# Kernel optimization log

Hardware: AMD Instinct MI355X
Metric: run time of the kernel (lower is better)

Reference implementation:

```python
import jax, jax.numpy as jnp
import numpy as np

BAND_LOW_MAX = 500.0
BAND_MID_MAX = 2000.0
ENERGY_THRESHOLD = 0.5

V, NH, NM = 1024, 16384, 16384


def setup_inputs() -> dict:
    key = jax.random.key(0)
    k1, k2, k3, k4, k5, k6 = jax.random.split(key, 6)
    harm_amps = jax.random.uniform(k1, (V, NH), dtype=jnp.float32)
    noise_mags = jax.random.uniform(k2, (V, NM), dtype=jnp.float32)
    # fundamental in [50, 1000) Hz so low/mid/high bands are all populated
    f0_hz = 50.0 + 950.0 * jax.random.uniform(k3, (V,), dtype=jnp.float32)
    competition_weight = 0.1 + jax.random.uniform(k4, (V,), dtype=jnp.float32)
    withdrawal = jax.random.uniform(k5, (V, 3), dtype=jnp.float32)  # [low, mid, high]
    is_active = jax.random.randint(k6, (V,), 0, 2).astype(bool)
    return {
        'harm_amps': harm_amps,
        'noise_mags': noise_mags,
        'f0_hz': f0_hz,
        'competition_weight': competition_weight,
        'withdrawal': withdrawal,
        'is_active': is_active,
    }


def reference(harm_amps, noise_mags, f0_hz, competition_weight, withdrawal, is_active):
    dt = harm_amps.dtype
    nh = harm_amps.shape[-1]
    actf = is_active.astype(dt)                     # [V]
    n_active = jnp.sum(is_active)

    harmonics = jnp.arange(1, nh + 1, dtype=dt)     # [NH]
    freqs = f0_hz[:, None] * harmonics[None, :]     # [V, NH]
    # bands partition the harmonics: 0=low (<500), 1=mid [500,2000), 2=high (>=2000)
    band_idx = (freqs >= BAND_LOW_MAX).astype(jnp.int32) + (freqs >= BAND_MID_MAX).astype(jnp.int32)  # [V, NH]

    # per-voice per-band energy (inactive voices contribute 0, as in the torch code)
    energy = jnp.stack(
        [jnp.sum(jnp.where(band_idx == b, harm_amps, jnp.zeros((), dt)), axis=-1) for b in range(3)],
        axis=1,
    ) * actf[:, None]                               # [V, 3]

    total_energy = jnp.sum(energy, axis=0)          # [3]
    total_weight = jnp.sum(competition_weight * actf)

    claim_ratio = competition_weight / jnp.maximum(total_weight, 1e-6)  # [V]
    my_share = claim_ratio * ENERGY_THRESHOLD                           # [V]
    excess = energy - my_share[:, None]                                 # [V, 3]
    excess_ratio = excess / jnp.maximum(energy, 1e-6)                   # [V, 3]
    reduction = jnp.maximum(0.3, 1.0 - withdrawal * excess_ratio * 0.5) # [V, 3]

    # reduction only applies when band is crowded, voice has energy, and voice exceeds its share
    apply = (total_energy[None, :] > ENERGY_THRESHOLD) & (energy > 0.0) & (excess > 0.0) & is_active[:, None]
    gain = jnp.where(apply, reduction, jnp.ones((), dt))                # [V, 3]

    elem_gain = jnp.take_along_axis(gain, band_idx, axis=1)             # [V, NH]
    harm_new = harm_amps * elem_gain

    total_before = jnp.sum(harm_amps, axis=-1)      # [V]
    total_after = jnp.sum(harm_new, axis=-1)        # [V]
    noise_scale = jnp.where(total_before > 1e-6, total_after / total_before, jnp.ones((), dt))
    noise_new = noise_mags * jnp.where(is_active, noise_scale, jnp.ones((), dt))[:, None]

    # inactive voices pass through unchanged
    harm_new = jnp.where(is_active[:, None], harm_new, harm_amps)

    # fewer than 2 active voices -> no competition at all
    changed = n_active >= 2
    harm_out = jnp.where(changed, harm_new, harm_amps)
    noise_out = jnp.where(changed, noise_new, noise_mags)
    # concat harm and noise outputs along last axis: [V, NH + NM]
    return jnp.concatenate([harm_out, noise_out], axis=-1)
```

## Files before the change

### kernel.cpp

```cpp
#include <hip/hip_runtime.h>

#define V   1024
#define NH  16384
#define NM  16384

#define BAND_LOW_MAX    500.0f
#define BAND_MID_MAX    2000.0f
#define ENERGY_THRESHOLD 0.5f

__global__ __launch_bounds__(256)
void pass1_band_energy(const float* __restrict__ harm,
                       const float* __restrict__ f0_hz,
                       float* __restrict__ Eraw ) {
    const int v = blockIdx.x;
    const float f0 = f0_hz[v];
    const float4* h4 = (const float4*)(harm + (size_t)v * NH);

    float e0 = 0.f, e1 = 0.f, e2 = 0.f;
    for (int c = threadIdx.x; c < NH / 4; c += blockDim.x) {
        float4 a = h4[c];
        const int hbase = c * 4;
        #pragma unroll
        for (int j = 0; j < 4; ++j) {
            float amp  = (&a.x)[j];
            float freq = f0 * (float)(hbase + j + 1);
            if (freq < BAND_LOW_MAX)       e0 += amp;
            else if (freq < BAND_MID_MAX)  e1 += amp;
            else                           e2 += amp;
        }
    }
    for (int off = 32; off > 0; off >>= 1) {
        e0 += __shfl_down(e0, off);
        e1 += __shfl_down(e1, off);
        e2 += __shfl_down(e2, off);
    }
    __shared__ float s[3][4];
    const int wid  = threadIdx.x >> 6;
    const int lane = threadIdx.x & 63;
    if (lane == 0) { s[0][wid] = e0; s[1][wid] = e1; s[2][wid] = e2; }
    __syncthreads();
    if (threadIdx.x == 0) {
        float t0 = 0.f, t1 = 0.f, t2 = 0.f;
        #pragma unroll
        for (int i = 0; i < 4; ++i) { t0 += s[0][i]; t1 += s[1][i]; t2 += s[2][i]; }
        Eraw[v * 3 + 0] = t0;
        Eraw[v * 3 + 1] = t1;
        Eraw[v * 3 + 2] = t2;
    }
}

__global__ __launch_bounds__(1024)
void pass2_gains(const float* __restrict__ Eraw,
                 const float* __restrict__ cw,
                 const float* __restrict__ wd,
                 const int*   __restrict__ is_active,
                 float* __restrict__ gains ) {
    const int v = threadIdx.x;
    const float e0 = Eraw[v * 3 + 0];
    const float e1 = Eraw[v * 3 + 1];
    const float e2 = Eraw[v * 3 + 2];
    const bool  act  = (is_active[v] != 0);
    const float actf = act ? 1.0f : 0.0f;
    const float w    = cw[v];

    const float ea0 = e0 * actf, ea1 = e1 * actf, ea2 = e2 * actf;

    float r0 = ea0, r1 = ea1, r2 = ea2, r3 = w * actf, r4 = actf;
    for (int off = 32; off > 0; off >>= 1) {
        r0 += __shfl_down(r0, off);
        r1 += __shfl_down(r1, off);
        r2 += __shfl_down(r2, off);
        r3 += __shfl_down(r3, off);
        r4 += __shfl_down(r4, off);
    }
    __shared__ float s[5][16];
    __shared__ float tot[5];
    const int wid  = threadIdx.x >> 6;
    const int lane = threadIdx.x & 63;
    if (lane == 0) {
        s[0][wid] = r0; s[1][wid] = r1; s[2][wid] = r2;
        s[3][wid] = r3; s[4][wid] = r4;
    }
    __syncthreads();
    if (threadIdx.x < 5) {
        float t = 0.f;
        #pragma unroll
        for (int i = 0; i < 16; ++i) t += s[threadIdx.x][i];
        tot[threadIdx.x] = t;
    }
    __syncthreads();

    const float TE0 = tot[0], TE1 = tot[1], TE2 = tot[2];
    const float TW  = tot[3];
    const bool changed = (tot[4] >= 1.5f);

    const float claim = w / fmaxf(TW, 1e-6f);
    const float share = claim * ENERGY_THRESHOLD;

    const float ea[3] = { ea0, ea1, ea2 };
    const float er[3] = { e0, e1, e2 };
    const float TE[3] = { TE0, TE1, TE2 };

    const float tbefore = e0 + e1 + e2;
    float tafter = 0.f;
    float g[3];
    #pragma unroll
    for (int b = 0; b < 3; ++b) {
        const float excess = ea[b] - share;
        const float exr    = excess / fmaxf(ea[b], 1e-6f);
        const float red    = fmaxf(0.3f, 1.0f - wd[v * 3 + b] * exr * 0.5f);
        const bool apply   = (TE[b] > ENERGY_THRESHOLD) && (ea[b] > 0.0f) &&
                             (excess > 0.0f) && act;
        const float gb = apply ? red : 1.0f;
        tafter += gb * er[b];
        g[b] = changed ? gb : 1.0f;
    }

    const float nscale = (tbefore > 1e-6f) ? (tafter / tbefore) : 1.0f;
    const float nse = (changed && act) ? nscale : 1.0f;

    gains[v * 4 + 0] = g[0];
    gains[v * 4 + 1] = g[1];
    gains[v * 4 + 2] = g[2];
    gains[v * 4 + 3] = nse;
}

__global__ __launch_bounds__(256)
void pass3_apply(const float* __restrict__ harm,
                 const float* __restrict__ noise,
                 const float* __restrict__ f0_hz,
                 const float* __restrict__ gains,
                 float* __restrict__ out) {
    const int idx = blockIdx.x * 256 + threadIdx.x;
    const int v = idx >> 13;
    const int c = idx & 8191;

    float4 o;
    if (c < 4096) {
        const float4 a = ((const float4*)harm)[(size_t)v * 4096 + c];
        const float f0 = f0_hz[v];
        const float g0 = gains[v * 4 + 0];
        const float g1 = gains[v * 4 + 1];
        const float g2 = gains[v * 4 + 2];
        const int hbase = c * 4;
        #pragma unroll
        for (int j = 0; j < 4; ++j) {
            const float freq = f0 * (float)(hbase + j + 1);
            const float g = (freq < BAND_LOW_MAX) ? g0
                          : (freq < BAND_MID_MAX) ? g1 : g2;
            (&o.x)[j] = (&a.x)[j] * g;
        }
    } else {
        const float4 nm = ((const float4*)noise)[(size_t)v * 4096 + (c - 4096)];
        const float ns = gains[v * 4 + 3];
        o.x = nm.x * ns; o.y = nm.y * ns; o.z = nm.z * ns; o.w = nm.w * ns;
    }
    ((float4*)out)[(size_t)v * 8192 + c] = o;
}

extern "C" void kernel_launch(void* const* d_in, const int* in_sizes, int n_in,
                              void* d_out, int out_size, void* d_ws, size_t ws_size,
                              hipStream_t stream) {
    const float* harm  = (const float*)d_in[0];
    const float* noise = (const float*)d_in[1];
    const float* f0    = (const float*)d_in[2];
    const float* cw    = (const float*)d_in[3];
    const float* wd    = (const float*)d_in[4];
    const int*   act   = (const int*)d_in[5];
    float* out = (float*)d_out;

    float* Eraw  = (float*)d_ws;
    float* gains = Eraw + 4096;

    pass1_band_energy<<<V, 256, 0, stream>>>(harm, f0, Eraw);
    pass2_gains<<<1, 1024, 0, stream>>>(Eraw, cw, wd, act, gains);

    const int n4 = V * 8192;
    pass3_apply<<<n4 / 256, 256, 0, stream>>>(harm, noise, f0, gains, out);
}
```

Baseline: 60.15 us.

## Fuse gain computation into apply kernel, dropping single-block reduction pass

Removes the serial single-block gains kernel. Each apply block now redundantly reduces the per-voice stats written by the first pass and computes its voice's band gains locally. Apply blocks each process a quarter-row slice of a voice with unrolled float4 loads and nontemporal stores, and pass1 is fully unrolled. This trades one launch and a serialized tiny kernel for redundant small L2 reads in every block.

```diff
diff --git a/kernel.cpp b/kernel.cpp
--- a/kernel.cpp
+++ b/kernel.cpp
@@ -8,25 +8,30 @@
 #define BAND_MID_MAX    2000.0f
 #define ENERGY_THRESHOLD 0.5f
 
+typedef float f32x4 __attribute__((ext_vector_type(4)));
+
 __global__ __launch_bounds__(256)
-void pass1_band_energy(const float* __restrict__ harm,
-                       const float* __restrict__ f0_hz,
-                       float* __restrict__ Eraw ) {
-    const int v = blockIdx.x;
+void k1_stats(const float* __restrict__ harm,
+              const float* __restrict__ f0_hz,
+              const float* __restrict__ cw,
+              const int*   __restrict__ is_active,
+              float* __restrict__ stats ) {
+    const int v   = blockIdx.x;
+    const int tid = threadIdx.x;
     const float f0 = f0_hz[v];
-    const float4* h4 = (const float4*)(harm + (size_t)v * NH);
+    const f32x4* hrow = (const f32x4*)harm + (size_t)v * 4096;
 
     float e0 = 0.f, e1 = 0.f, e2 = 0.f;
-    for (int c = threadIdx.x; c < NH / 4; c += blockDim.x) {
-        float4 a = h4[c];
-        const int hbase = c * 4;
+    #pragma unroll
+    for (int k = 0; k < 16; ++k) {
+        const f32x4 a = hrow[tid + k * 256];
+        const int hbase = (tid + k * 256) * 4;
         #pragma unroll
         for (int j = 0; j < 4; ++j) {
-            float amp  = (&a.x)[j];
-            float freq = f0 * (float)(hbase + j + 1);
-            if (freq < BAND_LOW_MAX)       e0 += amp;
-            else if (freq < BAND_MID_MAX)  e1 += amp;
-            else                           e2 += amp;
+            const float freq = f0 * (float)(hbase + j + 1);
+            if (freq < BAND_LOW_MAX)       e0 += a[j];
+            else if (freq < BAND_MID_MAX)  e1 += a[j];
+            else                           e2 += a[j];
         }
     }
     for (int off = 32; off > 0; off >>= 1) {
@@ -35,37 +40,48 @@
         e2 += __shfl_down(e2, off);
     }
     __shared__ float s[3][4];
-    const int wid  = threadIdx.x >> 6;
-    const int lane = threadIdx.x & 63;
+    const int wid  = tid >> 6;
+    const int lane = tid & 63;
     if (lane == 0) { s[0][wid] = e0; s[1][wid] = e1; s[2][wid] = e2; }
     __syncthreads();
-    if (threadIdx.x == 0) {
-        float t0 = 0.f, t1 = 0.f, t2 = 0.f;
-        #pragma unroll
-        for (int i = 0; i < 4; ++i) { t0 += s[0][i]; t1 += s[1][i]; t2 += s[2][i]; }
-        Eraw[v * 3 + 0] = t0;
-        Eraw[v * 3 + 1] = t1;
-        Eraw[v * 3 + 2] = t2;
+    if (tid == 0) {
+        const float t0 = s[0][0] + s[0][1] + s[0][2] + s[0][3];
+        const float t1 = s[1][0] + s[1][1] + s[1][2] + s[1][3];
+        const float t2 = s[2][0] + s[2][1] + s[2][2] + s[2][3];
+        const float af = (is_active[v] != 0) ? 1.0f : 0.0f;
+        stats[0 * V + v] = t0 * af;
+        stats[1 * V + v] = t1 * af;
+        stats[2 * V + v] = t2 * af;
+        stats[3 * V + v] = cw[v] * af;
+        stats[4 * V + v] = af;
     }
 }
 
-__global__ __launch_bounds__(1024)
-void pass2_gains(const float* __restrict__ Eraw,
-                 const float* __restrict__ cw,
-                 const float* __restrict__ wd,
-                 const int*   __restrict__ is_active,
-                 float* __restrict__ gains ) {
-    const int v = threadIdx.x;
-    const float e0 = Eraw[v * 3 + 0];
-    const float e1 = Eraw[v * 3 + 1];
-    const float e2 = Eraw[v * 3 + 2];
-    const bool  act  = (is_active[v] != 0);
-    const float actf = act ? 1.0f : 0.0f;
-    const float w    = cw[v];
+__global__ __launch_bounds__(256)
+void k2_apply(const float* __restrict__ harm,
+              const float* __restrict__ noise,
+              const float* __restrict__ f0_hz,
+              const float* __restrict__ cw,
+              const float* __restrict__ wd,
+              const int*   __restrict__ is_active,
+              const float* __restrict__ stats,
+              float* __restrict__ out) {
+    const int bid  = blockIdx.x;
+    const int v    = bid >> 3;
+    const int part = bid & 7;
+    const int tid  = threadIdx.x;
 
-    const float ea0 = e0 * actf, ea1 = e1 * actf, ea2 = e2 * actf;
-
-    float r0 = ea0, r1 = ea1, r2 = ea2, r3 = w * actf, r4 = actf;
+    const f32x4* sp = (const f32x4*)stats;
+    const f32x4 x0 = sp[0 * 256 + tid];
+    const f32x4 x1 = sp[1 * 256 + tid];
+    const f32x4 x2 = sp[2 * 256 + tid];
+    const f32x4 x3 = sp[3 * 256 + tid];
+    const f32x4 x4 = sp[4 * 256 + tid];
+    float r0 = (x0[0] + x0[1]) + (x0[2] + x0[3]);
+    float r1 = (x1[0] + x1[1]) + (x1[2] + x1[3]);
+    float r2 = (x2[0] + x2[1]) + (x2[2] + x2[3]);
+    float r3 = (x3[0] + x3[1]) + (x3[2] + x3[3]);
+    float r4 = (x4[0] + x4[1]) + (x4[2] + x4[3]);
     for (int off = 32; off > 0; off >>= 1) {
         r0 += __shfl_down(r0, off);
         r1 += __shfl_down(r1, off);
@@ -73,35 +89,29 @@
         r3 += __shfl_down(r3, off);
         r4 += __shfl_down(r4, off);
     }
-    __shared__ float s[5][16];
-    __shared__ float tot[5];
-    const int wid  = threadIdx.x >> 6;
-    const int lane = threadIdx.x & 63;
+    __shared__ float s2[5][4];
+    const int wid  = tid >> 6;
+    const int lane = tid & 63;
     if (lane == 0) {
-        s[0][wid] = r0; s[1][wid] = r1; s[2][wid] = r2;
-        s[3][wid] = r3; s[4][wid] = r4;
+        s2[0][wid] = r0; s2[1][wid] = r1; s2[2][wid] = r2;
+        s2[3][wid] = r3; s2[4][wid] = r4;
     }
     __syncthreads();
-    if (threadIdx.x < 5) {
-        float t = 0.f;
-        #pragma unroll
-        for (int i = 0; i < 16; ++i) t += s[threadIdx.x][i];
-        tot[threadIdx.x] = t;
-    }
-    __syncthreads();
+    const float TE[3] = {
+        s2[0][0] + s2[0][1] + s2[0][2] + s2[0][3],
+        s2[1][0] + s2[1][1] + s2[1][2] + s2[1][3],
+        s2[2][0] + s2[2][1] + s2[2][2] + s2[2][3] };
+    const float TW = s2[3][0] + s2[3][1] + s2[3][2] + s2[3][3];
+    const float NA = s2[4][0] + s2[4][1] + s2[4][2] + s2[4][3];
 
-    const float TE0 = tot[0], TE1 = tot[1], TE2 = tot[2];
-    const float TW  = tot[3];
-    const bool changed = (tot[4] >= 1.5f);
+    const bool  act     = (is_active[v] != 0);
+    const bool  changed = (NA >= 1.5f);
+    const float w       = cw[v];
+    const float share   = (w / fmaxf(TW, 1e-6f)) * ENERGY_THRESHOLD;
 
-    const float claim = w / fmaxf(TW, 1e-6f);
-    const float share = claim * ENERGY_THRESHOLD;
+    const float ea[3] = { stats[0 * V + v], stats[1 * V + v], stats[2 * V + v] };
 
-    const float ea[3] = { ea0, ea1, ea2 };
-    const float er[3] = { e0, e1, e2 };
-    const float TE[3] = { TE0, TE1, TE2 };
-
-    const float tbefore = e0 + e1 + e2;
+    const float tbefore = ea[0] + ea[1] + ea[2];
     float tafter = 0.f;
     float g[3];
     #pragma unroll
@@ -112,50 +122,42 @@
         const bool apply   = (TE[b] > ENERGY_THRESHOLD) && (ea[b] > 0.0f) &&
                              (excess > 0.0f) && act;
         const float gb = apply ? red : 1.0f;
-        tafter += gb * er[b];
+        tafter += gb * ea[b];
         g[b] = changed ? gb : 1.0f;
     }
+    const float nscale = (tbefore > 1e-6f) ? (tafter / tbefore) : 1.0f;
+    const float nse    = (changed && act) ? nscale : 1.0f;
+    const float g0 = g[0], g1 = g[1], g2 = g[2];
 
-    const float nscale = (tbefore > 1e-6f) ? (tafter / tbefore) : 1.0f;
-    const float nse = (changed && act) ? nscale : 1.0f;
-
-    gains[v * 4 + 0] = g[0];
-    gains[v * 4 + 1] = g[1];
-    gains[v * 4 + 2] = g[2];
-    gains[v * 4 + 3] = nse;
-}
-
-__global__ __launch_bounds__(256)
-void pass3_apply(const float* __restrict__ harm,
-                 const float* __restrict__ noise,
-                 const float* __restrict__ f0_hz,
-                 const float* __restrict__ gains,
-                 float* __restrict__ out) {
-    const int idx = blockIdx.x * 256 + threadIdx.x;
-    const int v = idx >> 13;
-    const int c = idx & 8191;
-
-    float4 o;
-    if (c < 4096) {
-        const float4 a = ((const float4*)harm)[(size_t)v * 4096 + c];
+    f32x4* orow = (f32x4*)out + (size_t)v * 8192;
+    if (part < 4) {
         const float f0 = f0_hz[v];
-        const float g0 = gains[v * 4 + 0];
-        const float g1 = gains[v * 4 + 1];
-        const float g2 = gains[v * 4 + 2];
-        const int hbase = c * 4;
+        const f32x4* hrow = (const f32x4*)harm + (size_t)v * 4096;
+        const int c0 = part * 1024 + tid;
         #pragma unroll
-        for (int j = 0; j < 4; ++j) {
-            const float freq = f0 * (float)(hbase + j + 1);
-            const float g = (freq < BAND_LOW_MAX) ? g0
-                          : (freq < BAND_MID_MAX) ? g1 : g2;
-            (&o.x)[j] = (&a.x)[j] * g;
+        for (int k = 0; k < 4; ++k) {
+            const int c = c0 + k * 256;
+            const f32x4 a = hrow[c];
+            f32x4 o;
+            #pragma unroll
+            for (int j = 0; j < 4; ++j) {
+                const float freq = f0 * (float)(c * 4 + j + 1);
+                const float gg = (freq < BAND_LOW_MAX) ? g0
+                               : (freq < BAND_MID_MAX) ? g1 : g2;
+                o[j] = a[j] * gg;
+            }
+            __builtin_nontemporal_store(o, orow + c);
         }
     } else {
-        const float4 nm = ((const float4*)noise)[(size_t)v * 4096 + (c - 4096)];
-        const float ns = gains[v * 4 + 3];
-        o.x = nm.x * ns; o.y = nm.y * ns; o.z = nm.z * ns; o.w = nm.w * ns;
+        const f32x4* nrow = (const f32x4*)noise + (size_t)v * 4096;
+        const int c0 = (part - 4) * 1024 + tid;
+        #pragma unroll
+        for (int k = 0; k < 4; ++k) {
+            const int c = c0 + k * 256;
+            const f32x4 n = nrow[c];
+            __builtin_nontemporal_store(n * nse, orow + 4096 + c);
+        }
     }
-    ((float4*)out)[(size_t)v * 8192 + c] = o;
 }
 
 extern "C" void kernel_launch(void* const* d_in, const int* in_sizes, int n_in,
@@ -167,14 +169,9 @@
     const float* cw    = (const float*)d_in[3];
     const float* wd    = (const float*)d_in[4];
     const int*   act   = (const int*)d_in[5];
-    float* out = (float*)d_out;
+    float* out   = (float*)d_out;
+    float* stats = (float*)d_ws;
 
-    float* Eraw  = (float*)d_ws;
-    float* gains = Eraw + 4096;
-
-    pass1_band_energy<<<V, 256, 0, stream>>>(harm, f0, Eraw);
-    pass2_gains<<<1, 1024, 0, stream>>>(Eraw, cw, wd, act, gains);
-
-    const int n4 = V * 8192;
-    pass3_apply<<<n4 / 256, 256, 0, stream>>>(harm, noise, f0, gains, out);
+    k1_stats<<<V, 256, 0, stream>>>(harm, f0, cw, act, stats);
+    k2_apply<<<V * 8, 256, 0, stream>>>(harm, noise, f0, cw, wd, act, stats, out);
 }
```

Measured after the change: 56.89 us. -5.4%, faster.
